# Kernel optimization log

Hardware: AMD Instinct MI355X
Metric: run time of the kernel (lower is better)

The kernel has to match this reference:

```python
import jax, jax.numpy as jnp
import numpy as np

HEAD_DIM = 64
MASK_PENALTY = 1000000.0


def setup_inputs() -> dict:
    key = jax.random.key(0)
    kq, kk, kv, ki = jax.random.split(key, 4)
    B, H, S, D = 32, 16, 512, HEAD_DIM
    E, CAP = 8, 4  # n_experts = hidden(1024)//128, capacity per expert
    Q = jax.random.normal(kq, (B, H, S, D), dtype=jnp.float32)
    K = jax.random.normal(kk, (B, H, S, D), dtype=jnp.float32)
    V = jax.random.normal(kv, (B, H, S, D), dtype=jnp.float32)
    idx_list = jax.random.randint(ki, (E, CAP), 0, B)  # per-expert routed batch indices
    mask = jnp.ones((B, S), dtype=jnp.float32)
    return {"Q": Q, "K": K, "V": V, "idx_list": idx_list, "mask": mask}


def reference(Q, K, V, idx_list, mask):
    # Per-expert grouped attention: gather routed batch rows, QK^T, masked
    # softmax, AV. Dropout is identity in eval mode.
    scale = 1.0 / jnp.sqrt(jnp.asarray(HEAD_DIM, dtype=Q.dtype))

    def expert_attn(idx_e):
        q = Q[idx_e]            # [cap, H, S, D]
        k = K[idx_e]
        v = V[idx_e]
        m = mask[idx_e]         # [cap, S]
        dot = jnp.einsum('bhsd,bhtd->bhst', q, k) * scale
        dot = dot - MASK_PENALTY * (1.0 - m[:, None, None, :])
        p = jax.nn.softmax(dot, axis=-1)
        return jnp.einsum('bhst,bhtd->bhsd', p, v)  # [cap, H, S, D]

    X = jax.vmap(expert_attn)(idx_list)  # [E, cap, H, S, D]
    return X
```

## Files before the change

### kernel.cpp

```cpp
#include <hip/hip_runtime.h>
#include <math.h>


typedef _Float16 f16x8 __attribute__((ext_vector_type(8)));
typedef _Float16 f16x4 __attribute__((ext_vector_type(4)));
typedef _Float16 f16x2 __attribute__((ext_vector_type(2)));
typedef float    f32x4 __attribute__((ext_vector_type(4)));

#define MFMA16(a, b, c) __builtin_amdgcn_mfma_f32_16x16x32_f16((a), (b), (c), 0, 0, 0)

constexpr int Hh = 16;
constexpr int Ss = 512;
constexpr int Dd = 64;
constexpr int QB = 128;
constexpr int KVB = 64;
constexpr float QS = 0.125f * 1.44269504088896f;
constexpr float BM = 1000000.0f * 1.44269504088896f;

union U4 { f16x4 v; f16x2 h[2]; };
union U8 { f16x8 v; f16x2 h[4]; };

__device__ __forceinline__ int SW(int row, int col) {
  return row * 64 + (col ^ ((row & 7) << 3));
}

__device__ __forceinline__ f16x2 pkrtz(float a, float b) {
  auto t = __builtin_amdgcn_cvt_pkrtz(a, b);
  return *(f16x2*)&t;
}

__global__ __launch_bounds__(256) void sparse_attn_kernel(
    const float* __restrict__ Q, const float* __restrict__ K,
    const float* __restrict__ V, const int* __restrict__ idx,
    const float* __restrict__ mask, float* __restrict__ out) {
  const int tid  = threadIdx.x;
  const int lane = tid & 63;
  const int wv   = tid >> 6;
  const int r    = lane & 15;
  const int g    = lane >> 4;

  const int phys = blockIdx.x;
  const int G    = (phys & 7) | ((phys >> 5) << 3);
  const int qb   = (phys >> 3) & 3;
  const int h    = G & 15;
  const int ec   = G >> 4;
  const int b    = idx[ec];

  __shared__ _Float16 Ks[64 * 64];
  __shared__ _Float16 VTs[64 * 64];
  __shared__ _Float16 Ps[4][32 * 64];
  __shared__ float    maskS[Ss];

  const size_t bh = ((size_t)b * Hh + h) * (size_t)Ss * Dd;
  const float* Qb = Q + bh;
  const float* Kb = K + bh;
  const float* Vb = V + bh;
  const float* mrow = mask + (size_t)b * Ss;

  *(float2*)&maskS[2 * tid] = *(const float2*)(mrow + 2 * tid);

  const int q0 = qb * QB + wv * 32;

  f16x8 qf[2][2];
#pragma unroll
  for (int mi = 0; mi < 2; ++mi)
#pragma unroll
    for (int kk = 0; kk < 2; ++kk) {
      const float* qp = Qb + (size_t)(q0 + mi * 16 + r) * Dd + kk * 32 + g * 8;
      float4 x0 = *(const float4*)qp;
      float4 x1 = *(const float4*)(qp + 4);
      U8 u;
      u.h[0] = pkrtz(x0.x * QS, x0.y * QS);
      u.h[1] = pkrtz(x0.z * QS, x0.w * QS);
      u.h[2] = pkrtz(x1.x * QS, x1.y * QS);
      u.h[3] = pkrtz(x1.z * QS, x1.w * QS);
      qf[mi][kk] = u.v;
    }

  f16x8 ones;
#pragma unroll
  for (int e = 0; e < 8; ++e) ones[e] = (_Float16)1.0f;

  f32x4 oacc[2][4];
#pragma unroll
  for (int mi = 0; mi < 2; ++mi)
#pragma unroll
    for (int nj = 0; nj < 4; ++nj) oacc[mi][nj] = (f32x4){0.f, 0.f, 0.f, 0.f};
  f32x4 lacc[2] = {(f32x4){0.f, 0.f, 0.f, 0.f}, (f32x4){0.f, 0.f, 0.f, 0.f}};

  float4 kx0[2], kx1[2];
  float  vv[2][8];

#define KV_ISSUE(KV0)                                                        \
  {                                                                          \
    _Pragma("unroll")                                                        \
    for (int it = 0; it < 2; ++it) {                                         \
      int j = it * 256 + tid;                                                \
      const float* kp_ = Kb + (size_t)((KV0) + (j >> 3)) * Dd + (j & 7) * 8; \
      kx0[it] = *(const float4*)kp_;                                         \
      kx1[it] = *(const float4*)(kp_ + 4);                                   \
    }                                                                        \
    _Pragma("unroll")                                                        \
    for (int it = 0; it < 2; ++it) {                                         \
      int oct = (tid >> 6) + 4 * it;                                         \
      const float* vp = Vb + (size_t)((KV0) + oct * 8) * Dd + (tid & 63);    \
      _Pragma("unroll")                                                      \
      for (int jj = 0; jj < 8; ++jj) vv[it][jj] = vp[(size_t)jj * Dd];       \
    }                                                                        \
  }

  KV_ISSUE(0)

  for (int t = 0; t < Ss / KVB; ++t) {
    const int kv0 = t * KVB;
    if (t) __syncthreads();

#pragma unroll
    for (int it = 0; it < 2; ++it) {
      int j = it * 256 + tid;
      U8 u;
      u.h[0] = pkrtz(kx0[it].x, kx0[it].y);
      u.h[1] = pkrtz(kx0[it].z, kx0[it].w);
      u.h[2] = pkrtz(kx1[it].x, kx1[it].y);
      u.h[3] = pkrtz(kx1[it].z, kx1[it].w);
      *(f16x8*)&Ks[SW(j >> 3, (j & 7) * 8)] = u.v;
    }
#pragma unroll
    for (int it = 0; it < 2; ++it) {
      int oct = (tid >> 6) + 4 * it;
      int dim = tid & 63;
      U8 u;
      u.h[0] = pkrtz(vv[it][0], vv[it][1]);
      u.h[1] = pkrtz(vv[it][2], vv[it][3]);
      u.h[2] = pkrtz(vv[it][4], vv[it][5]);
      u.h[3] = pkrtz(vv[it][6], vv[it][7]);
      *(f16x8*)&VTs[SW(dim, oct * 8)] = u.v;
    }
    __syncthreads();

    if (t < Ss / KVB - 1) KV_ISSUE(kv0 + KVB)

    f32x4 bv[4];
#pragma unroll
    for (int nj = 0; nj < 4; ++nj) {
      f32x4 mv = *(const f32x4*)&maskS[kv0 + nj * 16 + g * 4];
      bv[nj][0] = mv[0] * BM - BM;
      bv[nj][1] = mv[1] * BM - BM;
      bv[nj][2] = mv[2] * BM - BM;
      bv[nj][3] = mv[3] * BM - BM;
    }

    f32x4 sf[2][4];
#pragma unroll
    for (int nj = 0; nj < 4; ++nj) { sf[0][nj] = bv[nj]; sf[1][nj] = bv[nj]; }
    __builtin_amdgcn_s_setprio(1);
#pragma unroll
    for (int nj = 0; nj < 4; ++nj)
#pragma unroll
      for (int kk = 0; kk < 2; ++kk) {
        f16x8 kf = *(const f16x8*)&Ks[SW(nj * 16 + r, kk * 32 + g * 8)];
        sf[0][nj] = MFMA16(kf, qf[0][kk], sf[0][nj]);
        sf[1][nj] = MFMA16(kf, qf[1][kk], sf[1][nj]);
      }
    __builtin_amdgcn_s_setprio(0);

#pragma unroll
    for (int mi = 0; mi < 2; ++mi) {
      float p[4][4];
#pragma unroll
      for (int nj = 0; nj < 4; ++nj)
#pragma unroll
        for (int rg = 0; rg < 4; ++rg)
          p[nj][rg] = __builtin_amdgcn_exp2f(sf[mi][nj][rg]);

#pragma unroll
      for (int nj = 0; nj < 4; ++nj) {
        U4 w;
        w.h[0] = pkrtz(p[nj][0], p[nj][1]);
        w.h[1] = pkrtz(p[nj][2], p[nj][3]);
        *(f16x4*)&Ps[wv][SW(mi * 16 + r, nj * 16 + g * 4)] = w.v;
      }
    }

    __builtin_amdgcn_s_setprio(1);
#pragma unroll
    for (int kk = 0; kk < 2; ++kk) {
      f16x8 pf0 = *(const f16x8*)&Ps[wv][SW(r,      kk * 32 + g * 8)];
      f16x8 pf1 = *(const f16x8*)&Ps[wv][SW(16 + r, kk * 32 + g * 8)];
      lacc[0] = MFMA16(pf0, ones, lacc[0]);
      lacc[1] = MFMA16(pf1, ones, lacc[1]);
#pragma unroll
      for (int nj = 0; nj < 4; ++nj) {
        f16x8 vf = *(const f16x8*)&VTs[SW(nj * 16 + r, kk * 32 + g * 8)];
        oacc[0][nj] = MFMA16(pf0, vf, oacc[0][nj]);
        oacc[1][nj] = MFMA16(pf1, vf, oacc[1][nj]);
      }
    }
    __builtin_amdgcn_s_setprio(0);
  }

  float* ob = out + ((size_t)ec * Hh + h) * (size_t)Ss * Dd;
#pragma unroll
  for (int mi = 0; mi < 2; ++mi) {
    float i4[4];
#pragma unroll
    for (int rg = 0; rg < 4; ++rg) i4[rg] = 1.0f / lacc[mi][rg];
#pragma unroll
    for (int nj = 0; nj < 4; ++nj)
#pragma unroll
      for (int rg = 0; rg < 4; ++rg) {
        int row = q0 + mi * 16 + g * 4 + rg;
        int dim = nj * 16 + r;
        ob[(size_t)row * Dd + dim] = oacc[mi][nj][rg] * i4[rg];
      }
  }
}

extern "C" void kernel_launch(void* const* d_in, const int* in_sizes, int n_in,
                              void* d_out, int out_size, void* d_ws, size_t ws_size,
                              hipStream_t stream) {
  const float* Q    = (const float*)d_in[0];
  const float* K    = (const float*)d_in[1];
  const float* V    = (const float*)d_in[2];
  const int*   idx  = (const int*)d_in[3];
  const float* mask = (const float*)d_in[4];
  float* out = (float*)d_out;
  dim3 grid(2048), block(256);
  hipLaunchKernelGGL(sparse_attn_kernel, grid, block, 0, stream,
                     Q, K, V, idx, mask, out);
}
```

Before: 67.68 us.

## Keep softmax probabilities in registers by permuting V's key layout

Removes the per-wave shared-memory round trip for P by packing the exp2 outputs straight into MFMA A-operand fragments. To make the register layout of the QK^T accumulator line up with the PV operand, the key order in V^T shared memory is permuted to match when V is loaded. This drops LDS writes and reads plus 16KB of shared memory per block, which could raise occupancy. The V global loads now stride differently, which may affect coalescing only slightly.

```diff
diff --git a/kernel.cpp b/kernel.cpp
--- a/kernel.cpp
+++ b/kernel.cpp
@@ -17,7 +17,6 @@
 constexpr float QS = 0.125f * 1.44269504088896f;
 constexpr float BM = 1000000.0f * 1.44269504088896f;
 
-union U4 { f16x4 v; f16x2 h[2]; };
 union U8 { f16x8 v; f16x2 h[4]; };
 
 __device__ __forceinline__ int SW(int row, int col) {
@@ -48,7 +47,6 @@
 
   __shared__ _Float16 Ks[64 * 64];
   __shared__ _Float16 VTs[64 * 64];
-  __shared__ _Float16 Ps[4][32 * 64];
   __shared__ float    maskS[Ss];
 
   const size_t bh = ((size_t)b * Hh + h) * (size_t)Ss * Dd;
@@ -103,9 +101,13 @@
     _Pragma("unroll")                                                        \
     for (int it = 0; it < 2; ++it) {                                         \
       int oct = (tid >> 6) + 4 * it;                                         \
-      const float* vp = Vb + (size_t)((KV0) + oct * 8) * Dd + (tid & 63);    \
+      int kb1 = (oct >> 2) * 16 + (oct & 3) * 4;                             \
+      const float* vp = Vb + (size_t)((KV0) + kb1) * Dd + (tid & 63);        \
       _Pragma("unroll")                                                      \
-      for (int jj = 0; jj < 8; ++jj) vv[it][jj] = vp[(size_t)jj * Dd];       \
+      for (int jj = 0; jj < 4; ++jj) {                                       \
+        vv[it][jj]     = vp[(size_t)jj * Dd];                                \
+        vv[it][jj + 4] = vp[(size_t)(jj + 32) * Dd];                         \
+      }                                                                      \
     }                                                                        \
   }
 
@@ -164,6 +166,7 @@
       }
     __builtin_amdgcn_s_setprio(0);
 
+    f16x8 pf[2][2];
 #pragma unroll
     for (int mi = 0; mi < 2; ++mi) {
       float p[4][4];
@@ -172,28 +175,27 @@
 #pragma unroll
         for (int rg = 0; rg < 4; ++rg)
           p[nj][rg] = __builtin_amdgcn_exp2f(sf[mi][nj][rg]);
-
-#pragma unroll
-      for (int nj = 0; nj < 4; ++nj) {
-        U4 w;
-        w.h[0] = pkrtz(p[nj][0], p[nj][1]);
-        w.h[1] = pkrtz(p[nj][2], p[nj][3]);
-        *(f16x4*)&Ps[wv][SW(mi * 16 + r, nj * 16 + g * 4)] = w.v;
+#pragma unroll
+      for (int kk = 0; kk < 2; ++kk) {
+        U8 u;
+        u.h[0] = pkrtz(p[kk][0], p[kk][1]);
+        u.h[1] = pkrtz(p[kk][2], p[kk][3]);
+        u.h[2] = pkrtz(p[kk + 2][0], p[kk + 2][1]);
+        u.h[3] = pkrtz(p[kk + 2][2], p[kk + 2][3]);
+        pf[mi][kk] = u.v;
       }
     }
 
     __builtin_amdgcn_s_setprio(1);
 #pragma unroll
     for (int kk = 0; kk < 2; ++kk) {
-      f16x8 pf0 = *(const f16x8*)&Ps[wv][SW(r,      kk * 32 + g * 8)];
-      f16x8 pf1 = *(const f16x8*)&Ps[wv][SW(16 + r, kk * 32 + g * 8)];
-      lacc[0] = MFMA16(pf0, ones, lacc[0]);
-      lacc[1] = MFMA16(pf1, ones, lacc[1]);
+      lacc[0] = MFMA16(pf[0][kk], ones, lacc[0]);
+      lacc[1] = MFMA16(pf[1][kk], ones, lacc[1]);
 #pragma unroll
       for (int nj = 0; nj < 4; ++nj) {
         f16x8 vf = *(const f16x8*)&VTs[SW(nj * 16 + r, kk * 32 + g * 8)];
-        oacc[0][nj] = MFMA16(pf0, vf, oacc[0][nj]);
-        oacc[1][nj] = MFMA16(pf1, vf, oacc[1][nj]);
+        oacc[0][nj] = MFMA16(pf[0][kk], vf, oacc[0][nj]);
+        oacc[1][nj] = MFMA16(pf[1][kk], vf, oacc[1][nj]);
       }
     }
     __builtin_amdgcn_s_setprio(0);
```

After: 64.98 us. -4.0%, faster.
